# Kernel tuning notes

Measured on AMD Instinct MI355X. Metric: run time of the kernel, lower is better.

## Reference

```python
import jax, jax.numpy as jnp
import numpy as np

B, S, DM, H, SD = 8, 2048, 512, 8, 64
INNER = H * SD
HID = 4 * DM
EPS = 1e-5


def setup_inputs() -> dict:
    key = jax.random.key(0)
    ks = jax.random.split(key, 12)
    p = lambda k, sh: jax.random.normal(k, sh, dtype=jnp.float32) * 0.02
    return {
        "x": jax.random.normal(ks[0], (B, S, DM), dtype=jnp.float32),
        "norm_g": jnp.ones((DM,), jnp.float32),
        "norm_b": jnp.zeros((DM,), jnp.float32),
        "ffn_norm_g": jnp.ones((DM,), jnp.float32),
        "ffn_norm_b": jnp.zeros((DM,), jnp.float32),
        "Wa": p(ks[1], (INNER, DM)),
        "Wb": p(ks[2], (INNER, DM)),
        "Wql": p(ks[3], (INNER, DM)),
        "Wqr": p(ks[4], (INNER, DM)),
        "Wsd": p(ks[5], (H, DM)),
        "bsd": jnp.zeros((H,), jnp.float32),
        "Wpd": p(ks[6], (H, DM)),
        "bpd": jnp.zeros((H,), jnp.float32),
        "Wout": p(ks[7], (DM, INNER)),
        "W1": p(ks[8], (HID, DM)),
        "b1": jnp.zeros((HID,), jnp.float32),
        "W2": p(ks[9], (DM, HID)),
        "b2": jnp.zeros((DM,), jnp.float32),
    }


def _ln(x, g, b):
    m = x.mean(-1, keepdims=True)
    v = ((x - m) ** 2).mean(-1, keepdims=True)
    return (x - m) / jnp.sqrt(v + EPS) * g + b


def reference(x, norm_g, norm_b, ffn_norm_g, ffn_norm_b, Wa, Wb, Wql, Wqr,
              Wsd, bsd, Wpd, bpd, Wout, W1, b1, W2, b2):
    n = _ln(x, norm_g, norm_b)  # [B,S,DM]
    # project, reshape to heads, move time axis first for scan: [S,B,H,SD]
    tm = lambda t: t.reshape(B, S, H, SD).transpose(1, 0, 2, 3)
    a_all = tm(jnp.tanh(n @ Wa.T))
    b_all = tm(jnp.tanh(n @ Wb.T))
    ql_all = tm(jnp.tanh(n @ Wql.T))
    qr_all = tm(jnp.tanh(n @ Wqr.T))
    sd_all = jax.nn.sigmoid(n @ Wsd.T + bsd).transpose(1, 0, 2)[..., None]        # [S,B,H,1]
    pd_all = jax.nn.sigmoid(n @ Wpd.T + bpd).transpose(1, 0, 2)[..., None, None]  # [S,B,H,1,1]

    def step(carry, inp):
        state, pair = carry  # state [B,H,SD], pair [B,H,SD,SD]
        at, bt, qlt, sdt, pdt = inp
        prev = state
        state = sdt * state + (1.0 - sdt) * at
        pair = pdt * pair + (1.0 - pdt) * jnp.einsum('bhd,bhe->bhde', prev, bt)
        lc = jnp.einsum('bhde,bhd->bhe', pair, qlt)  # left context [B,H,SD]
        return (state, pair), lc

    init = (jnp.zeros((B, H, SD), x.dtype), jnp.zeros((B, H, SD, SD), x.dtype))
    _, lc = jax.lax.scan(step, init, (a_all, b_all, ql_all, sd_all, pd_all))  # [S,B,H,SD]

    mixed = ((lc * qr_all).transpose(1, 0, 2, 3).reshape(B, S, INNER)) @ Wout.T  # [B,S,DM]
    r = x + mixed  # dropout is identity in eval
    h = jax.nn.gelu(_ln(r, ffn_norm_g, ffn_norm_b) @ W1.T + b1, approximate=False)
    return r + h @ W2.T + b2
```

## Files before the change

### kernel.cpp

```cpp
#include <hip/hip_runtime.h>
#include <cstdint>
#include <cstddef>

#define B_    8
#define S_    2048
#define DM_   512
#define H_    8
#define SD_   64
#define HID_  2048
#define ROWS  (B_*S_)
#define BH    (B_*H_)
#define NCHUNK 32
#define CLEN   64
#define EPS_  1e-5f
#define PLANE ((size_t)ROWS*64)

typedef __bf16 bf16x8 __attribute__((ext_vector_type(8)));
typedef float  floatx4 __attribute__((ext_vector_type(4)));


static __device__ __forceinline__ float bf2f(unsigned short h){
  union { unsigned int u; float f; } v; v.u = ((unsigned int)h) << 16; return v.f;
}
static __device__ __forceinline__ unsigned short f2bf(float f){
  union { float f; unsigned int u; } v; v.f = f;
  unsigned int r = v.u + 0x7fffu + ((v.u >> 16) & 1u);
  return (unsigned short)(r >> 16);
}
static __device__ __forceinline__ float fast_tanh(float x){
  float ax = fabsf(x);
  float e  = __expf(2.f*ax);
  float t  = 1.f - 2.f/(e+1.f);
  return copysignf(t, x);
}
static __device__ __forceinline__ float sigmoidf_(float z){
  return 1.f/(1.f + expf(-z));
}
static __device__ __forceinline__ float gelu_exact(float x){
  return 0.5f*x*(1.f + erff(x*0.70710678118654752440f));
}
static __device__ __forceinline__ void gld_lds16(const unsigned short* g, unsigned short* lds){
  __builtin_amdgcn_global_load_lds(
      (const __attribute__((address_space(1))) void*)g,
      (__attribute__((address_space(3))) void*)lds,
      16, 0, 0);
}
static __device__ __forceinline__ int swz(int row, int col){
  return row*64 + (((col>>3) ^ (row&7))<<3) + (col&7);
}

__global__ __launch_bounds__(256) void cvt_weights(
    const float* __restrict__ wa, const float* __restrict__ wb,
    const float* __restrict__ wql, const float* __restrict__ wqr,
    const float* __restrict__ wout, const float* __restrict__ w1,
    const float* __restrict__ w2,
    unsigned short* __restrict__ wcat, unsigned short* __restrict__ woutb,
    unsigned short* __restrict__ w1b, unsigned short* __restrict__ w2b){
  int i = blockIdx.x*256 + threadIdx.x;
  const float* s; unsigned short* d; int base;
  if      (i <  65536){ s=wa;   d=wcat;          base=i; }
  else if (i < 131072){ s=wb;   d=wcat+262144;   base=i-65536; }
  else if (i < 196608){ s=wql;  d=wcat+524288;   base=i-131072; }
  else if (i < 262144){ s=wqr;  d=wcat+786432;   base=i-196608; }
  else if (i < 327680){ s=wout; d=woutb;         base=i-262144; }
  else if (i < 589824){ s=w1;   d=w1b;           base=i-327680; }
  else                { s=w2;   d=w2b;           base=i-589824; }
  float4 v = ((const float4*)s)[base];
  ushort4 o; o.x=f2bf(v.x); o.y=f2bf(v.y); o.z=f2bf(v.z); o.w=f2bf(v.w);
  ((ushort4*)d)[base] = o;
}

__global__ __launch_bounds__(256) void ln_gates(
    const float* __restrict__ x, const float* __restrict__ gam, const float* __restrict__ bet,
    const float* __restrict__ Wsd, const float* __restrict__ bsd,
    const float* __restrict__ Wpd, const float* __restrict__ bpd,
    unsigned short* __restrict__ nbf, float* __restrict__ sdo, float* __restrict__ pdo){
  const int row = blockIdx.x*4 + (threadIdx.x>>6), l = threadIdx.x & 63;
  const float* xr = x + (size_t)row*DM_;
  float4 v0 = ((const float4*)xr)[l*2];
  float4 v1 = ((const float4*)xr)[l*2+1];
  float v[8] = {v0.x,v0.y,v0.z,v0.w,v1.x,v1.y,v1.z,v1.w};
  float s = 0.f;
  #pragma unroll
  for (int i=0;i<8;++i) s += v[i];
  #pragma unroll
  for (int m=1;m<64;m<<=1) s += __shfl_xor(s, m);
  const float mean = s * (1.f/512.f);
  float q = 0.f;
  #pragma unroll
  for (int i=0;i<8;++i){ float d = v[i]-mean; q += d*d; }
  #pragma unroll
  for (int m=1;m<64;m<<=1) q += __shfl_xor(q, m);
  const float rstd = rsqrtf(q*(1.f/512.f) + EPS_);
  float4 g0 = ((const float4*)gam)[l*2], g1 = ((const float4*)gam)[l*2+1];
  float4 b0 = ((const float4*)bet)[l*2], b1 = ((const float4*)bet)[l*2+1];
  float gg[8] = {g0.x,g0.y,g0.z,g0.w,g1.x,g1.y,g1.z,g1.w};
  float bb[8] = {b0.x,b0.y,b0.z,b0.w,b1.x,b1.y,b1.z,b1.w};
  float n[8];
  #pragma unroll
  for (int i=0;i<8;++i) n[i] = (v[i]-mean)*rstd*gg[i] + bb[i];
  ushort4 o0, o1;
  o0.x=f2bf(n[0]); o0.y=f2bf(n[1]); o0.z=f2bf(n[2]); o0.w=f2bf(n[3]);
  o1.x=f2bf(n[4]); o1.y=f2bf(n[5]); o1.z=f2bf(n[6]); o1.w=f2bf(n[7]);
  ((ushort4*)(nbf + (size_t)row*DM_))[l*2]   = o0;
  ((ushort4*)(nbf + (size_t)row*DM_))[l*2+1] = o1;
  float acc[16];
  #pragma unroll
  for (int hh=0; hh<8; ++hh){
    const float4* ws = (const float4*)(Wsd + hh*DM_) + l*2;
    const float4* wp = (const float4*)(Wpd + hh*DM_) + l*2;
    float4 a0=ws[0], a1=ws[1], p0=wp[0], p1=wp[1];
    acc[hh]   = n[0]*a0.x+n[1]*a0.y+n[2]*a0.z+n[3]*a0.w+n[4]*a1.x+n[5]*a1.y+n[6]*a1.z+n[7]*a1.w;
    acc[8+hh] = n[0]*p0.x+n[1]*p0.y+n[2]*p0.z+n[3]*p0.w+n[4]*p1.x+n[5]*p1.y+n[6]*p1.z+n[7]*p1.w;
  }
  #pragma unroll
  for (int k=0;k<16;++k){
    float a = acc[k];
    #pragma unroll
    for (int m=1;m<64;m<<=1) a += __shfl_xor(a, m);
    acc[k] = a;
  }
  if (l==0){
    #pragma unroll
    for (int hh=0; hh<8; ++hh){
      sdo[row*8+hh] = sigmoidf_(acc[hh]   + bsd[hh]);
      pdo[row*8+hh] = sigmoidf_(acc[8+hh] + bpd[hh]);
    }
  }
}

__global__ __launch_bounds__(256) void ln_plain(
    const unsigned short* __restrict__ xb, const float* __restrict__ gam, const float* __restrict__ bet,
    unsigned short* __restrict__ ob){
  const int row = blockIdx.x*4 + (threadIdx.x>>6), l = threadIdx.x & 63;
  const unsigned short* xr = xb + (size_t)row*DM_ + l*8;
  ushort4 u0 = *(const ushort4*)xr;
  ushort4 u1 = *(const ushort4*)(xr+4);
  float v[8] = {bf2f(u0.x),bf2f(u0.y),bf2f(u0.z),bf2f(u0.w),
                bf2f(u1.x),bf2f(u1.y),bf2f(u1.z),bf2f(u1.w)};
  float s = 0.f;
  #pragma unroll
  for (int i=0;i<8;++i) s += v[i];
  #pragma unroll
  for (int m=1;m<64;m<<=1) s += __shfl_xor(s, m);
  const float mean = s * (1.f/512.f);
  float q = 0.f;
  #pragma unroll
  for (int i=0;i<8;++i){ float d = v[i]-mean; q += d*d; }
  #pragma unroll
  for (int m=1;m<64;m<<=1) q += __shfl_xor(q, m);
  const float rstd = rsqrtf(q*(1.f/512.f) + EPS_);
  float4 g0 = ((const float4*)gam)[l*2], g1 = ((const float4*)gam)[l*2+1];
  float4 b0 = ((const float4*)bet)[l*2], b1 = ((const float4*)bet)[l*2+1];
  float gg[8] = {g0.x,g0.y,g0.z,g0.w,g1.x,g1.y,g1.z,g1.w};
  float bb[8] = {b0.x,b0.y,b0.z,b0.w,b1.x,b1.y,b1.z,b1.w};
  ushort4 o0, o1;
  o0.x=f2bf((v[0]-mean)*rstd*gg[0]+bb[0]); o0.y=f2bf((v[1]-mean)*rstd*gg[1]+bb[1]);
  o0.z=f2bf((v[2]-mean)*rstd*gg[2]+bb[2]); o0.w=f2bf((v[3]-mean)*rstd*gg[3]+bb[3]);
  o1.x=f2bf((v[4]-mean)*rstd*gg[4]+bb[4]); o1.y=f2bf((v[5]-mean)*rstd*gg[5]+bb[5]);
  o1.z=f2bf((v[6]-mean)*rstd*gg[6]+bb[6]); o1.w=f2bf((v[7]-mean)*rstd*gg[7]+bb[7]);
  ((ushort4*)(ob + (size_t)row*DM_))[l*2]   = o0;
  ((ushort4*)(ob + (size_t)row*DM_))[l*2+1] = o1;
}

template<int MODE>
__global__ __launch_bounds__(256) void gemm128(
    const unsigned short* __restrict__ A, const unsigned short* __restrict__ W,
    const float* __restrict__ bias, const float* __restrict__ residf,
    const unsigned short* __restrict__ residb,
    float* __restrict__ outf, unsigned short* __restrict__ outb,
    int N, int K){
  __shared__ __align__(16) unsigned short As[128*64];
  __shared__ __align__(16) unsigned short Ws[128*64];
  const int tid  = threadIdx.x;
  const int w    = tid >> 6;
  const int lane = tid & 63;
  const int mblk = blockIdx.x, nblk = blockIdx.y;
  const int mrow = (w >> 1) * 64;
  const int ncol = (w & 1) * 64;
  const int fr = lane & 15, fq = lane >> 4;

  int srow[4], scol[4];
  #pragma unroll
  for (int q=0;q<4;++q){
    const int p = q*256 + w*64 + lane;
    srow[q] = p >> 3;
    scol[q] = ((p & 7) ^ (srow[q] & 7)) * 8;
  }

  floatx4 acc[4][4];
  #pragma unroll
  for (int i=0;i<4;++i)
    #pragma unroll
    for (int j=0;j<4;++j)
      acc[i][j] = (floatx4){0.f,0.f,0.f,0.f};

  for (int k0=0; k0<K; k0+=64){
    #pragma unroll
    for (int q=0;q<4;++q){
      gld_lds16(A + (size_t)(mblk*128 + srow[q])*K + k0 + scol[q], As + (q*256 + w*64)*8);
      gld_lds16(W + (size_t)(nblk*128 + srow[q])*K + k0 + scol[q], Ws + (q*256 + w*64)*8);
    }
    __syncthreads();
    #pragma unroll
    for (int kh=0;kh<2;++kh){
      bf16x8 af[4], bf[4];
      #pragma unroll
      for (int i=0;i<4;++i) af[i] = *(const bf16x8*)&As[swz(mrow + i*16 + fr, kh*32 + fq*8)];
      #pragma unroll
      for (int j=0;j<4;++j) bf[j] = *(const bf16x8*)&Ws[swz(ncol + j*16 + fr, kh*32 + fq*8)];
      #pragma unroll
      for (int i=0;i<4;++i)
        #pragma unroll
        for (int j=0;j<4;++j)
          acc[i][j] = __builtin_amdgcn_mfma_f32_16x16x32_bf16(af[i], bf[j], acc[i][j], 0, 0, 0);
    }
    __syncthreads();
  }

  #pragma unroll
  for (int i=0;i<4;++i){
    const int grow_base = mblk*128 + mrow + i*16 + fq*4;
    #pragma unroll
    for (int j=0;j<4;++j){
      const int gcol = nblk*128 + ncol + j*16 + fr;
      float bias_v = 0.f;
      if (MODE==2 || MODE==3) bias_v = bias[gcol];
      #pragma unroll
      for (int r=0;r<4;++r){
        float v = acc[i][j][r];
        if (MODE==0){
          const size_t o = (size_t)(gcol>>6)*PLANE + (size_t)(grow_base + r)*64 + (gcol & 63);
          outb[o] = f2bf(fast_tanh(v));
        } else {
          const size_t o = (size_t)(grow_base + r)*N + gcol;
          if      (MODE==1) outb[o] = f2bf(residf[o] + v);
          else if (MODE==2) outb[o] = f2bf(gelu_exact(v + bias_v));
          else              outf[o] = bf2f(residb[o]) + v + bias_v;
        }
      }
    }
  }
}

__global__ __launch_bounds__(64) void state_local(
    const unsigned short* __restrict__ proj, const float* __restrict__ sdo,
    unsigned short* __restrict__ slocb, float* __restrict__ Sarr,
    float* __restrict__ sEnd){
  __shared__ __align__(16) unsigned short a_s[4096];
  __shared__ float sv_s[64];
  const int c = blockIdx.x, bh = blockIdx.y, b = bh>>3, h = bh&7, d = threadIdx.x;
  const int t0 = c*CLEN;
  const unsigned short* ap = proj + (size_t)h*PLANE + (size_t)(b*S_+t0)*64;
  #pragma unroll
  for (int q=0;q<8;++q)
    *(float4*)&a_s[(q*64 + d)*8] = *(const float4*)(ap + (size_t)(q*64 + d)*8);
  sv_s[d] = sdo[(b*S_+t0+d)*8 + h];
  __syncthreads();
  float s = 0.f, S = 1.f;
  #pragma unroll 4
  for (int j=0;j<CLEN;++j){
    const int t = t0 + j;
    float a  = bf2f(a_s[j*64 + d]);
    float sv = sv_s[j];
    s = sv*s + (1.f-sv)*a;
    S *= sv;
    slocb[((size_t)bh*S_ + t)*64 + d] = f2bf(s);
    if (d==0) Sarr[bh*S_ + t] = S;
  }
  sEnd[((size_t)c*BH + bh)*64 + d] = s;
}

__global__ __launch_bounds__(64) void state_combine(
    const float* __restrict__ sEnd, const float* __restrict__ Sarr,
    float* __restrict__ sinit){
  const int bh = blockIdx.x, d = threadIdx.x;
  float acc = 0.f;
  for (int c=0;c<NCHUNK;++c){
    sinit[((size_t)c*BH + bh)*64 + d] = acc;
    const int te = c*CLEN + CLEN - 1;
    acc = Sarr[bh*S_ + te]*acc + sEnd[((size_t)c*BH + bh)*64 + d];
  }
}

__global__ __launch_bounds__(64) void pair_localm(
    const unsigned short* __restrict__ proj, const float* __restrict__ pdo,
    const unsigned short* __restrict__ slocb, const float* __restrict__ Sarr,
    const float* __restrict__ sinit, float* __restrict__ pairbuf,
    float* __restrict__ Dprod){
  __shared__ __align__(16) unsigned short Bt[4096];
  __shared__ __align__(16) unsigned short Pt[4096];
  const int c=blockIdx.x, bh=blockIdx.y, b=bh>>3, h=bh&7, l=threadIdx.x;
  const int t = c*CLEN + l;
  float pd = pdo[(b*S_+t)*8 + h];
  float D = pd;
  #pragma unroll
  for (int m=1;m<64;m<<=1){ float o = __shfl_up(D, m); if (l>=m) D *= o; }
  const float Dend = __shfl(D, 63);
  const float cu = (Dend / D) * (1.f - pd);
  if (l==63) Dprod[c*BH+bh] = Dend;
  {
    const unsigned short* brow = proj + (size_t)(8+h)*PLANE + (size_t)(b*S_+t)*64;
    const size_t ptm = (size_t)bh*S_ + (l==0 ? t : t-1);
    const unsigned short* srow = slocb + ptm*64;
    const float* initp = sinit + ((size_t)c*BH + bh)*64;
    float sp = 0.f;
    if (l>0) sp = Sarr[ptm];
    #pragma unroll
    for (int e8=0;e8<8;++e8){
      ushort4 u0 = *(const ushort4*)(brow + e8*8);
      ushort4 u1 = *(const ushort4*)(brow + e8*8 + 4);
      unsigned short vs[8] = {u0.x,u0.y,u0.z,u0.w,u1.x,u1.y,u1.z,u1.w};
      ushort4 s0 = *(const ushort4*)(srow + e8*8);
      ushort4 s1 = *(const ushort4*)(srow + e8*8 + 4);
      unsigned short ss[8] = {s0.x,s0.y,s0.z,s0.w,s1.x,s1.y,s1.z,s1.w};
      float4 i0 = *(const float4*)(initp + e8*8);
      float4 i1 = *(const float4*)(initp + e8*8 + 4);
      float iv[8] = {i0.x,i0.y,i0.z,i0.w,i1.x,i1.y,i1.z,i1.w};
      #pragma unroll
      for (int q=0;q<8;++q){
        const int r = e8*8+q;
        float p = (l==0) ? iv[q] : (sp*iv[q] + bf2f(ss[q]));
        Bt[swz(r, l)] = f2bf(cu * bf2f(vs[q]));
        Pt[swz(r, l)] = f2bf(p);
      }
    }
  }
  __syncthreads();
  const int fr = l & 15, fq = l >> 4;
  floatx4 acc[4][4];
  #pragma unroll
  for (int i=0;i<4;++i)
    #pragma unroll
    for (int j=0;j<4;++j) acc[i][j] = (floatx4){0.f,0.f,0.f,0.f};
  #pragma unroll
  for (int kh=0;kh<2;++kh){
    bf16x8 af[4], bfr[4];
    #pragma unroll
    for (int i=0;i<4;++i) af[i]  = *(const bf16x8*)&Bt[swz(i*16+fr, kh*32+fq*8)];
    #pragma unroll
    for (int j=0;j<4;++j) bfr[j] = *(const bf16x8*)&Pt[swz(j*16+fr, kh*32+fq*8)];
    #pragma unroll
    for (int i=0;i<4;++i)
      #pragma unroll
      for (int j=0;j<4;++j)
        acc[i][j] = __builtin_amdgcn_mfma_f32_16x16x32_bf16(af[i], bfr[j], acc[i][j], 0, 0, 0);
  }
  float* outp = pairbuf + ((size_t)c*BH + bh)*4096;
  #pragma unroll
  for (int i=0;i<4;++i)
    #pragma unroll
    for (int j=0;j<4;++j)
      #pragma unroll
      for (int r=0;r<4;++r)
        outp[(i*16+fq*4+r)*64 + j*16+fr] = acc[i][j][r];
}

__global__ __launch_bounds__(256) void pair_combine(
    const float* __restrict__ pairbuf, const float* __restrict__ Dprod,
    unsigned short* __restrict__ pinitb){
  const int idx = blockIdx.x*256 + threadIdx.x;
  const int de = idx & 4095, bh = idx >> 12;
  float acc = 0.f;
  for (int c=0;c<NCHUNK;++c){
    const size_t o = ((size_t)c*BH + bh)*4096 + de;
    pinitb[o] = f2bf(acc);
    acc = Dprod[c*BH + bh]*acc + pairbuf[o];
  }
}

__global__ __launch_bounds__(64) void pair_finalm(
    const unsigned short* __restrict__ proj, const float* __restrict__ pdo,
    const unsigned short* __restrict__ slocb, const float* __restrict__ Sarr,
    const float* __restrict__ sinit, const unsigned short* __restrict__ pinitb,
    unsigned short* __restrict__ lcqr){
  __shared__ __align__(16) unsigned short Bt[4096];
  __shared__ __align__(16) unsigned short Tb[4096];
  __shared__ __align__(16) float Dtl[64];
  __shared__ __align__(16) float cudl[64];
  const int c=blockIdx.x, bh=blockIdx.y, b=bh>>3, h=bh&7, l=threadIdx.x;
  const int t0 = c*CLEN;
  const int trow = t0 + l;
  float pd = pdo[(b*S_+trow)*8 + h];
  float D = pd;
  #pragma unroll
  for (int m=1;m<64;m<<=1){ float o = __shfl_up(D, m); if (l>=m) D *= o; }
  Dtl[l]  = D;
  cudl[l] = (1.f - pd) / D;
  {
    const unsigned short* brow = proj + (size_t)(8+h)*PLANE + (size_t)(b*S_+trow)*64;
    #pragma unroll
    for (int e8=0;e8<8;++e8){
      ushort4 u0 = *(const ushort4*)(brow + e8*8);
      ushort4 u1 = *(const ushort4*)(brow + e8*8 + 4);
      unsigned short vs[8] = {u0.x,u0.y,u0.z,u0.w,u1.x,u1.y,u1.z,u1.w};
      #pragma unroll
      for (int q=0;q<8;++q) Bt[swz(e8*8+q, l)] = vs[q];
    }
  }
  __syncthreads();
  const int fr = l & 15, fq = l >> 4;
  const float* initp = sinit + ((size_t)c*BH + bh)*64;
  bf16x8 qf[4][2], pf[4][2];
  #pragma unroll
  for (int i=0;i<4;++i){
    const int tr = t0 + i*16 + fr;
    const bool first = (i==0 && fr==0);
    const size_t ptm = (size_t)bh*S_ + (first ? tr : tr-1);
    float sp = 0.f;
    if (!first) sp = Sarr[ptm];
    #pragma unroll
    for (int kh=0;kh<2;++kh){
      qf[i][kh] = *(const bf16x8*)(proj + (size_t)(16+h)*PLANE + (size_t)(b*S_ + tr)*64 + kh*32 + fq*8);
      bf16x8 sv = *(const bf16x8*)(slocb + ptm*64 + kh*32 + fq*8);
      float4 i0 = *(const float4*)(initp + kh*32 + fq*8);
      float4 i1 = *(const float4*)(initp + kh*32 + fq*8 + 4);
      float iv[8] = {i0.x,i0.y,i0.z,i0.w,i1.x,i1.y,i1.z,i1.w};
      bf16x8 pv;
      #pragma unroll
      for (int e=0;e<8;++e){
        float p = first ? iv[e] : (sp*iv[e] + (float)sv[e]);
        pv[e] = (__bf16)p;
      }
      pf[i][kh] = pv;
    }
  }
  floatx4 sacc[4][4];
  #pragma unroll
  for (int i=0;i<4;++i)
    #pragma unroll
    for (int j=0;j<4;++j) sacc[i][j] = (floatx4){0.f,0.f,0.f,0.f};
  #pragma unroll
  for (int kh=0;kh<2;++kh)
    #pragma unroll
    for (int i=0;i<4;++i)
      #pragma unroll
      for (int j=0;j<4;++j)
        sacc[i][j] = __builtin_amdgcn_mfma_f32_16x16x32_bf16(qf[i][kh], pf[j][kh], sacc[i][j], 0, 0, 0);
  float mycud[4];
  #pragma unroll
  for (int j=0;j<4;++j) mycud[j] = cudl[j*16+fr];
  #pragma unroll
  for (int i=0;i<4;++i){
    floatx4 dtv = *(const floatx4*)&Dtl[i*16+fq*4];
    #pragma unroll
    for (int j=0;j<4;++j){
      const int uu = j*16+fr;
      #pragma unroll
      for (int r=0;r<4;++r){
        const int tt = i*16+fq*4+r;
        float v = (uu<=tt) ? (sacc[i][j][r]*dtv[r])*mycud[j] : 0.f;
        Tb[swz(tt, uu)] = f2bf(v);
      }
    }
  }
  __syncthreads();
  floatx4 acc[4][4];
  #pragma unroll
  for (int i=0;i<4;++i)
    #pragma unroll
    for (int j=0;j<4;++j) acc[i][j] = (floatx4){0.f,0.f,0.f,0.f};
  #pragma unroll
  for (int kh=0;kh<2;++kh){
    bf16x8 af[4], bfr[4];
    #pragma unroll
    for (int i=0;i<4;++i) af[i]  = *(const bf16x8*)&Tb[swz(i*16+fr, kh*32+fq*8)];
    #pragma unroll
    for (int j=0;j<4;++j) bfr[j] = *(const bf16x8*)&Bt[swz(j*16+fr, kh*32+fq*8)];
    #pragma unroll
    for (int i=0;i<4;++i)
      #pragma unroll
      for (int j=0;j<4;++j)
        acc[i][j] = __builtin_amdgcn_mfma_f32_16x16x32_bf16(af[i], bfr[j], acc[i][j], 0, 0, 0);
  }
  {
    const unsigned short* ib = pinitb + ((size_t)c*BH + bh)*4096;
    #pragma unroll
    for (int kh=0;kh<2;++kh){
      bf16x8 qs[4], inf[4];
      #pragma unroll
      for (int i=0;i<4;++i){
        const float sc = Dtl[i*16+fr];
        #pragma unroll
        for (int e=0;e<8;++e) qs[i][e] = (__bf16)(sc * (float)qf[i][kh][e]);
      }
      #pragma unroll
      for (int j=0;j<4;++j)
        inf[j] = *(const bf16x8*)(ib + (j*16+fr)*64 + kh*32 + fq*8);
      #pragma unroll
      for (int i=0;i<4;++i)
        #pragma unroll
        for (int j=0;j<4;++j)
          acc[i][j] = __builtin_amdgcn_mfma_f32_16x16x32_bf16(qs[i], inf[j], acc[i][j], 0, 0, 0);
    }
  }
  __syncthreads();
  #pragma unroll
  for (int i=0;i<4;++i)
    #pragma unroll
    for (int j=0;j<4;++j)
      #pragma unroll
      for (int r=0;r<4;++r)
        Tb[swz(i*16+fq*4+r, j*16+fr)] = f2bf(acc[i][j][r]);
  __syncthreads();
  {
    const unsigned short* qrow = proj + (size_t)(24+h)*PLANE + (size_t)(b*S_+trow)*64;
    unsigned short* orow = lcqr + ((size_t)(b*S_+trow))*512 + h*64;
    #pragma unroll
    for (int e8=0;e8<8;++e8){
      bf16x8 lcv = *(const bf16x8*)&Tb[swz(l, e8*8)];
      ushort4 q0 = *(const ushort4*)(qrow + e8*8);
      ushort4 q1 = *(const ushort4*)(qrow + e8*8 + 4);
      unsigned short qv[8] = {q0.x,q0.y,q0.z,q0.w,q1.x,q1.y,q1.z,q1.w};
      ushort4 o0, o1;
      o0.x = f2bf((float)lcv[0]*bf2f(qv[0]));
      o0.y = f2bf((float)lcv[1]*bf2f(qv[1]));
      o0.z = f2bf((float)lcv[2]*bf2f(qv[2]));
      o0.w = f2bf((float)lcv[3]*bf2f(qv[3]));
      o1.x = f2bf((float)lcv[4]*bf2f(qv[4]));
      o1.y = f2bf((float)lcv[5]*bf2f(qv[5]));
      o1.z = f2bf((float)lcv[6]*bf2f(qv[6]));
      o1.w = f2bf((float)lcv[7]*bf2f(qv[7]));
      *(ushort4*)(orow + e8*8)     = o0;
      *(ushort4*)(orow + e8*8 + 4) = o1;
    }
  }
}

extern "C" void kernel_launch(void* const* d_in, const int* in_sizes, int n_in,
                              void* d_out, int out_size, void* d_ws, size_t ws_size,
                              hipStream_t stream){
  (void)in_sizes; (void)n_in; (void)out_size; (void)ws_size;
  const float* x    = (const float*)d_in[0];
  const float* ng   = (const float*)d_in[1];
  const float* nb   = (const float*)d_in[2];
  const float* fng  = (const float*)d_in[3];
  const float* fnb  = (const float*)d_in[4];
  const float* Wa   = (const float*)d_in[5];
  const float* Wb   = (const float*)d_in[6];
  const float* Wql  = (const float*)d_in[7];
  const float* Wqr  = (const float*)d_in[8];
  const float* Wsd  = (const float*)d_in[9];
  const float* bsd  = (const float*)d_in[10];
  const float* Wpd  = (const float*)d_in[11];
  const float* bpd  = (const float*)d_in[12];
  const float* Wout = (const float*)d_in[13];
  const float* W1   = (const float*)d_in[14];
  const float* b1   = (const float*)d_in[15];
  const float* W2   = (const float*)d_in[16];
  const float* b2   = (const float*)d_in[17];
  float* out = (float*)d_out;
  char* ws = (char*)d_ws;

  size_t off = 0;
  auto alloc = [&](size_t bytes)->char*{ char* p = ws + off; off += (bytes + 255) & ~(size_t)255; return p; };
  char* RA = alloc((size_t)ROWS*DM_*2);
  char* RB = alloc((size_t)ROWS*2048*2);
  char* RD = alloc((size_t)NCHUNK*BH*4096*4);
  char* RE = alloc((size_t)BH*S_*64*4);
  float* sdo   = (float*)alloc((size_t)ROWS*8*4);
  float* pdo   = (float*)alloc((size_t)ROWS*8*4);
  float* Sarr  = (float*)alloc((size_t)BH*S_*4);
  float* sinit = (float*)alloc((size_t)NCHUNK*BH*64*4);
  float* sEnd  = (float*)alloc((size_t)NCHUNK*BH*64*4);
  float* dprod = (float*)alloc((size_t)NCHUNK*BH*4);
  unsigned short* wcat  = (unsigned short*)alloc((size_t)2048*512*2);
  unsigned short* woutb = (unsigned short*)alloc((size_t)512*512*2);
  unsigned short* w1b   = (unsigned short*)alloc((size_t)2048*512*2);
  unsigned short* w2b   = (unsigned short*)alloc((size_t)512*2048*2);

  unsigned short* nbf   = (unsigned short*)RA;
  unsigned short* lcqr  = (unsigned short*)RA;
  unsigned short* nr    = (unsigned short*)RA;
  unsigned short* proj  = (unsigned short*)RB;
  unsigned short* hbuf  = (unsigned short*)RB;
  float* pairb = (float*)RD;
  unsigned short* slocb  = (unsigned short*)RE;
  unsigned short* rbufb  = (unsigned short*)RE;
  unsigned short* pinitb = (unsigned short*)(RE + (size_t)BH*S_*64*2);

  cvt_weights<<<dim3(3328), dim3(256), 0, stream>>>(Wa,Wb,Wql,Wqr,Wout,W1,W2, wcat,woutb,w1b,w2b);
  ln_gates<<<dim3(ROWS/4), dim3(256), 0, stream>>>(x, ng, nb, Wsd, bsd, Wpd, bpd, nbf, sdo, pdo);
  gemm128<0><<<dim3(128,16), dim3(256), 0, stream>>>(nbf, wcat, nullptr, nullptr, nullptr, nullptr, proj, 2048, 512);
  state_local<<<dim3(NCHUNK,BH), dim3(64), 0, stream>>>(proj, sdo, slocb, Sarr, sEnd);
  state_combine<<<dim3(BH), dim3(64), 0, stream>>>(sEnd, Sarr, sinit);
  pair_localm<<<dim3(NCHUNK,BH), dim3(64), 0, stream>>>(proj, pdo, slocb, Sarr, sinit, pairb, dprod);
  pair_combine<<<dim3(1024), dim3(256), 0, stream>>>(pairb, dprod, pinitb);
  pair_finalm<<<dim3(NCHUNK,BH), dim3(64), 0, stream>>>(proj, pdo, slocb, Sarr, sinit, pinitb, lcqr);
  gemm128<1><<<dim3(128,4), dim3(256), 0, stream>>>(lcqr, woutb, nullptr, x, nullptr, nullptr, rbufb, 512, 512);
  ln_plain<<<dim3(ROWS/4), dim3(256), 0, stream>>>(rbufb, fng, fnb, nr);
  gemm128<2><<<dim3(128,16), dim3(256), 0, stream>>>(nr, w1b, b1, nullptr, nullptr, nullptr, hbuf, 2048, 512);
  gemm128<3><<<dim3(128,4), dim3(256), 0, stream>>>(hbuf, w2b, b2, nullptr, rbufb, out, nullptr, 512, 2048);
}
```

Baseline: 407.0 us.

## Split chunked pair-scan kernels across two waves and transpose gate layout

```diff
diff --git a/kernel.cpp b/kernel.cpp
--- a/kernel.cpp
+++ b/kernel.cpp
@@ -123,8 +123,8 @@
   if (l==0){
     #pragma unroll
     for (int hh=0; hh<8; ++hh){
-      sdo[row*8+hh] = sigmoidf_(acc[hh]   + bsd[hh]);
-      pdo[row*8+hh] = sigmoidf_(acc[8+hh] + bpd[hh]);
+      sdo[(size_t)hh*ROWS + row] = sigmoidf_(acc[hh]   + bsd[hh]);
+      pdo[(size_t)hh*ROWS + row] = sigmoidf_(acc[8+hh] + bpd[hh]);
     }
   }
 }
@@ -255,7 +255,7 @@
   #pragma unroll
   for (int q=0;q<8;++q)
     *(float4*)&a_s[(q*64 + d)*8] = *(const float4*)(ap + (size_t)(q*64 + d)*8);
-  sv_s[d] = sdo[(b*S_+t0+d)*8 + h];
+  sv_s[d] = sdo[(size_t)h*ROWS + b*S_+t0+d];
   __syncthreads();
   float s = 0.f, S = 1.f;
   #pragma unroll 4
@@ -283,22 +283,23 @@
   }
 }
 
-__global__ __launch_bounds__(64) void pair_localm(
+__global__ __launch_bounds__(128) void pair_localm(
     const unsigned short* __restrict__ proj, const float* __restrict__ pdo,
     const unsigned short* __restrict__ slocb, const float* __restrict__ Sarr,
     const float* __restrict__ sinit, float* __restrict__ pairbuf,
     float* __restrict__ Dprod){
   __shared__ __align__(16) unsigned short Bt[4096];
   __shared__ __align__(16) unsigned short Pt[4096];
-  const int c=blockIdx.x, bh=blockIdx.y, b=bh>>3, h=bh&7, l=threadIdx.x;
+  const int c=blockIdx.x, bh=blockIdx.y, b=bh>>3, h=bh&7;
+  const int w = threadIdx.x>>6, l = threadIdx.x&63;
   const int t = c*CLEN + l;
-  float pd = pdo[(b*S_+t)*8 + h];
+  float pd = pdo[(size_t)h*ROWS + b*S_+t];
   float D = pd;
   #pragma unroll
   for (int m=1;m<64;m<<=1){ float o = __shfl_up(D, m); if (l>=m) D *= o; }
   const float Dend = __shfl(D, 63);
   const float cu = (Dend / D) * (1.f - pd);
-  if (l==63) Dprod[c*BH+bh] = Dend;
+  if (w==0 && l==63) Dprod[c*BH+bh] = Dend;
   {
     const unsigned short* brow = proj + (size_t)(8+h)*PLANE + (size_t)(b*S_+t)*64;
     const size_t ptm = (size_t)bh*S_ + (l==0 ? t : t-1);
@@ -307,7 +308,7 @@
     float sp = 0.f;
     if (l>0) sp = Sarr[ptm];
     #pragma unroll
-    for (int e8=0;e8<8;++e8){
+    for (int e8=w*4; e8<w*4+4; ++e8){
       ushort4 u0 = *(const ushort4*)(brow + e8*8);
       ushort4 u1 = *(const ushort4*)(brow + e8*8 + 4);
       unsigned short vs[8] = {u0.x,u0.y,u0.z,u0.w,u1.x,u1.y,u1.z,u1.w};
@@ -328,32 +329,32 @@
   }
   __syncthreads();
   const int fr = l & 15, fq = l >> 4;
-  floatx4 acc[4][4];
+  floatx4 acc[4][2];
   #pragma unroll
   for (int i=0;i<4;++i)
     #pragma unroll
-    for (int j=0;j<4;++j) acc[i][j] = (floatx4){0.f,0.f,0.f,0.f};
+    for (int jj=0;jj<2;++jj) acc[i][jj] = (floatx4){0.f,0.f,0.f,0.f};
   #pragma unroll
   for (int kh=0;kh<2;++kh){
-    bf16x8 af[4], bfr[4];
-    #pragma unroll
-    for (int i=0;i<4;++i) af[i]  = *(const bf16x8*)&Bt[swz(i*16+fr, kh*32+fq*8)];
-    #pragma unroll
-    for (int j=0;j<4;++j) bfr[j] = *(const bf16x8*)&Pt[swz(j*16+fr, kh*32+fq*8)];
+    bf16x8 af[4], bfr[2];
+    #pragma unroll
+    for (int i=0;i<4;++i)  af[i]  = *(const bf16x8*)&Bt[swz(i*16+fr, kh*32+fq*8)];
+    #pragma unroll
+    for (int jj=0;jj<2;++jj) bfr[jj] = *(const bf16x8*)&Pt[swz((w*2+jj)*16+fr, kh*32+fq*8)];
     #pragma unroll
     for (int i=0;i<4;++i)
       #pragma unroll
-      for (int j=0;j<4;++j)
-        acc[i][j] = __builtin_amdgcn_mfma_f32_16x16x32_bf16(af[i], bfr[j], acc[i][j], 0, 0, 0);
+      for (int jj=0;jj<2;++jj)
+        acc[i][jj] = __builtin_amdgcn_mfma_f32_16x16x32_bf16(af[i], bfr[jj], acc[i][jj], 0, 0, 0);
   }
   float* outp = pairbuf + ((size_t)c*BH + bh)*4096;
   #pragma unroll
   for (int i=0;i<4;++i)
     #pragma unroll
-    for (int j=0;j<4;++j)
+    for (int jj=0;jj<2;++jj)
       #pragma unroll
       for (int r=0;r<4;++r)
-        outp[(i*16+fq*4+r)*64 + j*16+fr] = acc[i][j][r];
+        outp[(i*16+fq*4+r)*64 + (w*2+jj)*16+fr] = acc[i][jj][r];
 }
 
 __global__ __launch_bounds__(256) void pair_combine(
@@ -369,7 +370,7 @@
   }
 }
 
-__global__ __launch_bounds__(64) void pair_finalm(
+__global__ __launch_bounds__(128) void pair_finalm(
     const unsigned short* __restrict__ proj, const float* __restrict__ pdo,
     const unsigned short* __restrict__ slocb, const float* __restrict__ Sarr,
     const float* __restrict__ sinit, const unsigned short* __restrict__ pinitb,
@@ -378,19 +379,19 @@
   __shared__ __align__(16) unsigned short Tb[4096];
   __shared__ __align__(16) float Dtl[64];
   __shared__ __align__(16) float cudl[64];
-  const int c=blockIdx.x, bh=blockIdx.y, b=bh>>3, h=bh&7, l=threadIdx.x;
+  const int c=blockIdx.x, bh=blockIdx.y, b=bh>>3, h=bh&7;
+  const int w=threadIdx.x>>6, l=threadIdx.x&63;
   const int t0 = c*CLEN;
   const int trow = t0 + l;
-  float pd = pdo[(b*S_+trow)*8 + h];
+  float pd = pdo[(size_t)h*ROWS + b*S_+trow];
   float D = pd;
   #pragma unroll
   for (int m=1;m<64;m<<=1){ float o = __shfl_up(D, m); if (l>=m) D *= o; }
-  Dtl[l]  = D;
-  cudl[l] = (1.f - pd) / D;
+  if (w==0){ Dtl[l] = D; cudl[l] = (1.f - pd) / D; }
   {
     const unsigned short* brow = proj + (size_t)(8+h)*PLANE + (size_t)(b*S_+trow)*64;
     #pragma unroll
-    for (int e8=0;e8<8;++e8){
+    for (int e8=w*4; e8<w*4+4; ++e8){
       ushort4 u0 = *(const ushort4*)(brow + e8*8);
       ushort4 u1 = *(const ushort4*)(brow + e8*8 + 4);
       unsigned short vs[8] = {u0.x,u0.y,u0.z,u0.w,u1.x,u1.y,u1.z,u1.w};
@@ -401,17 +402,22 @@
   __syncthreads();
   const int fr = l & 15, fq = l >> 4;
   const float* initp = sinit + ((size_t)c*BH + bh)*64;
-  bf16x8 qf[4][2], pf[4][2];
-  #pragma unroll
-  for (int i=0;i<4;++i){
-    const int tr = t0 + i*16 + fr;
-    const bool first = (i==0 && fr==0);
+  bf16x8 qf[4][2], pf[2][2];
+  #pragma unroll
+  for (int i=0;i<4;++i)
+    #pragma unroll
+    for (int kh=0;kh<2;++kh)
+      qf[i][kh] = *(const bf16x8*)(proj + (size_t)(16+h)*PLANE + (size_t)(b*S_ + t0 + i*16 + fr)*64 + kh*32 + fq*8);
+  #pragma unroll
+  for (int jw=0;jw<2;++jw){
+    const int jx = w*2+jw;
+    const int tr = t0 + jx*16 + fr;
+    const bool first = (jx==0 && fr==0);
     const size_t ptm = (size_t)bh*S_ + (first ? tr : tr-1);
     float sp = 0.f;
     if (!first) sp = Sarr[ptm];
     #pragma unroll
     for (int kh=0;kh<2;++kh){
-      qf[i][kh] = *(const bf16x8*)(proj + (size_t)(16+h)*PLANE + (size_t)(b*S_ + tr)*64 + kh*32 + fq*8);
       bf16x8 sv = *(const bf16x8*)(slocb + ptm*64 + kh*32 + fq*8);
       float4 i0 = *(const float4*)(initp + kh*32 + fq*8);
       float4 i1 = *(const float4*)(initp + kh*32 + fq*8 + 4);
@@ -422,62 +428,62 @@
         float p = first ? iv[e] : (sp*iv[e] + (float)sv[e]);
         pv[e] = (__bf16)p;
       }
-      pf[i][kh] = pv;
-    }
-  }
-  floatx4 sacc[4][4];
+      pf[jw][kh] = pv;
+    }
+  }
+  floatx4 sacc[4][2];
   #pragma unroll
   for (int i=0;i<4;++i)
     #pragma unroll
-    for (int j=0;j<4;++j) sacc[i][j] = (floatx4){0.f,0.f,0.f,0.f};
+    for (int jw=0;jw<2;++jw) sacc[i][jw] = (floatx4){0.f,0.f,0.f,0.f};
   #pragma unroll
   for (int kh=0;kh<2;++kh)
     #pragma unroll
     for (int i=0;i<4;++i)
       #pragma unroll
-      for (int j=0;j<4;++j)
-        sacc[i][j] = __builtin_amdgcn_mfma_f32_16x16x32_bf16(qf[i][kh], pf[j][kh], sacc[i][j], 0, 0, 0);
-  float mycud[4];
-  #pragma unroll
-  for (int j=0;j<4;++j) mycud[j] = cudl[j*16+fr];
+      for (int jw=0;jw<2;++jw)
+        sacc[i][jw] = __builtin_amdgcn_mfma_f32_16x16x32_bf16(qf[i][kh], pf[jw][kh], sacc[i][jw], 0, 0, 0);
+  float mycud[2];
+  #pragma unroll
+  for (int jw=0;jw<2;++jw) mycud[jw] = cudl[(w*2+jw)*16+fr];
   #pragma unroll
   for (int i=0;i<4;++i){
     floatx4 dtv = *(const floatx4*)&Dtl[i*16+fq*4];
     #pragma unroll
-    for (int j=0;j<4;++j){
-      const int uu = j*16+fr;
+    for (int jw=0;jw<2;++jw){
+      const int uu = (w*2+jw)*16+fr;
       #pragma unroll
       for (int r=0;r<4;++r){
         const int tt = i*16+fq*4+r;
-        float v = (uu<=tt) ? (sacc[i][j][r]*dtv[r])*mycud[j] : 0.f;
+        float v = (uu<=tt) ? (sacc[i][jw][r]*dtv[r])*mycud[jw] : 0.f;
         Tb[swz(tt, uu)] = f2bf(v);
       }
     }
   }
   __syncthreads();
-  floatx4 acc[4][4];
+  floatx4 acc[4][2];
   #pragma unroll
   for (int i=0;i<4;++i)
     #pragma unroll
-    for (int j=0;j<4;++j) acc[i][j] = (floatx4){0.f,0.f,0.f,0.f};
+    for (int jw=0;jw<2;++jw) acc[i][jw] = (floatx4){0.f,0.f,0.f,0.f};
   #pragma unroll
   for (int kh=0;kh<2;++kh){
-    bf16x8 af[4], bfr[4];
-    #pragma unroll
-    for (int i=0;i<4;++i) af[i]  = *(const bf16x8*)&Tb[swz(i*16+fr, kh*32+fq*8)];
-    #pragma unroll
-    for (int j=0;j<4;++j) bfr[j] = *(const bf16x8*)&Bt[swz(j*16+fr, kh*32+fq*8)];
+    bf16x8 af[4], bfr[2];
+    #pragma unroll
+    for (int i=0;i<4;++i)  af[i]  = *(const bf16x8*)&Tb[swz(i*16+fr, kh*32+fq*8)];
+    #pragma unroll
+    for (int jw=0;jw<2;++jw) bfr[jw] = *(const bf16x8*)&Bt[swz((w*2+jw)*16+fr, kh*32+fq*8)];
     #pragma unroll
     for (int i=0;i<4;++i)
       #pragma unroll
-      for (int j=0;j<4;++j)
-        acc[i][j] = __builtin_amdgcn_mfma_f32_16x16x32_bf16(af[i], bfr[j], acc[i][j], 0, 0, 0);
+      for (int jw=0;jw<2;++jw)
+        acc[i][jw] = __builtin_amdgcn_mfma_f32_16x16x32_bf16(af[i], bfr[jw], acc[i][jw], 0, 0, 0);
   }
   {
     const unsigned short* ib = pinitb + ((size_t)c*BH + bh)*4096;
     #pragma unroll
     for (int kh=0;kh<2;++kh){
-      bf16x8 qs[4], inf[4];
+      bf16x8 qs[4], inf[2];
       #pragma unroll
       for (int i=0;i<4;++i){
         const float sc = Dtl[i*16+fr];
@@ -485,29 +491,29 @@
         for (int e=0;e<8;++e) qs[i][e] = (__bf16)(sc * (float)qf[i][kh][e]);
       }
       #pragma unroll
-      for (int j=0;j<4;++j)
-        inf[j] = *(const bf16x8*)(ib + (j*16+fr)*64 + kh*32 + fq*8);
+      for (int jw=0;jw<2;++jw)
+        inf[jw] = *(const bf16x8*)(ib + ((w*2+jw)*16+fr)*64 + kh*32 + fq*8);
       #pragma unroll
       for (int i=0;i<4;++i)
         #pragma unroll
-        for (int j=0;j<4;++j)
-          acc[i][j] = __builtin_amdgcn_mfma_f32_16x16x32_bf16(qs[i], inf[j], acc[i][j], 0, 0, 0);
+        for (int jw=0;jw<2;++jw)
+          acc[i][jw] = __builtin_amdgcn_mfma_f32_16x16x32_bf16(qs[i], inf[jw], acc[i][jw], 0, 0, 0);
     }
   }
   __syncthreads();
   #pragma unroll
   for (int i=0;i<4;++i)
     #pragma unroll
-    for (int j=0;j<4;++j)
+    for (int jw=0;jw<2;++jw)
       #pragma unroll
       for (int r=0;r<4;++r)
-        Tb[swz(i*16+fq*4+r, j*16+fr)] = f2bf(acc[i][j][r]);
+        Tb[swz(i*16+fq*4+r, (w*2+jw)*16+fr)] = f2bf(acc[i][jw][r]);
   __syncthreads();
   {
     const unsigned short* qrow = proj + (size_t)(24+h)*PLANE + (size_t)(b*S_+trow)*64;
     unsigned short* orow = lcqr + ((size_t)(b*S_+trow))*512 + h*64;
     #pragma unroll
-    for (int e8=0;e8<8;++e8){
+    for (int e8=w*4; e8<w*4+4; ++e8){
       bf16x8 lcv = *(const bf16x8*)&Tb[swz(l, e8*8)];
       ushort4 q0 = *(const ushort4*)(qrow + e8*8);
       ushort4 q1 = *(const ushort4*)(qrow + e8*8 + 4);
@@ -584,9 +590,9 @@
   gemm128<0><<<dim3(128,16), dim3(256), 0, stream>>>(nbf, wcat, nullptr, nullptr, nullptr, nullptr, proj, 2048, 512);
   state_local<<<dim3(NCHUNK,BH), dim3(64), 0, stream>>>(proj, sdo, slocb, Sarr, sEnd);
   state_combine<<<dim3(BH), dim3(64), 0, stream>>>(sEnd, Sarr, sinit);
-  pair_localm<<<dim3(NCHUNK,BH), dim3(64), 0, stream>>>(proj, pdo, slocb, Sarr, sinit, pairb, dprod);
+  pair_localm<<<dim3(NCHUNK,BH), dim3(128), 0, stream>>>(proj, pdo, slocb, Sarr, sinit, pairb, dprod);
   pair_combine<<<dim3(1024), dim3(256), 0, stream>>>(pairb, dprod, pinitb);
-  pair_finalm<<<dim3(NCHUNK,BH), dim3(64), 0, stream>>>(proj, pdo, slocb, Sarr, sinit, pinitb, lcqr);
+  pair_finalm<<<dim3(NCHUNK,BH), dim3(128), 0, stream>>>(proj, pdo, slocb, Sarr, sinit, pinitb, lcqr);
   gemm128<1><<<dim3(128,4), dim3(256), 0, stream>>>(lcqr, woutb, nullptr, x, nullptr, nullptr, rbufb, 512, 512);
   ln_plain<<<dim3(ROWS/4), dim3(256), 0, stream>>>(rbufb, fng, fnb, nr);
   gemm128<2><<<dim3(128,16), dim3(256), 0, stream>>>(nr, w1b, b1, nullptr, nullptr, nullptr, hbuf, 2048, 512);
```

Result: no change. 404.0 us (-0.7%).
